# Optimization experiments

Measured on AMD Instinct MI355X. Metric: run time of the kernel, lower is better.

Reference implementation:

```python
import jax, jax.numpy as jnp
import numpy as np


def setup_inputs() -> dict:
    key = jax.random.key(0)
    k1, k2 = jax.random.split(key)
    s = jax.random.normal(k1, (8192, 512), dtype=jnp.float32)
    t = jax.random.normal(k2, (8192, 512), dtype=jnp.float32)
    return {"s": s, "t": t}


def reference(s, t):
    # Pairwise squared Euclidean distance: dist[i, j] = ||t[j] - s[i]||^2
    # Expressed via the identity ||s||^2 + ||t||^2 - 2 s @ t^T to avoid
    # materializing the [n, q, d] broadcast intermediate of the original.
    s_sq = jnp.sum(s * s, axis=1)  # [n]
    t_sq = jnp.sum(t * t, axis=1)  # [q]
    cross = jnp.einsum('nd,qd->nq', s, t)  # [n, q]
    dist = s_sq[:, None] + t_sq[None, :] - 2.0 * cross
    return dist
```

## Files before the change

### kernel.cpp

```cpp
#include <hip/hip_runtime.h>
#include <hip/hip_bf16.h>
#include <stdint.h>


typedef __attribute__((ext_vector_type(8))) short short8v;
typedef __attribute__((ext_vector_type(4))) float f32x4;

static __device__ __forceinline__ unsigned short f32_to_bf16_rne(float f) {
    unsigned int u = __float_as_uint(f);
    unsigned int lsb = (u >> 16) & 1u;
    u += 0x7fffu + lsb;
    return (unsigned short)(u >> 16);
}

static __device__ __forceinline__ void async_load16(const void* g, void* l) {
    __builtin_amdgcn_global_load_lds(
        (const __attribute__((address_space(1))) void*)g,
        (__attribute__((address_space(3))) void*)l,
        16, 0, 0);
}

__global__ __launch_bounds__(256) void prep_kernel(const float* __restrict__ x,
                                                   unsigned short* __restrict__ xb,
                                                   float* __restrict__ nrm,
                                                   float scale) {
    const int tid  = threadIdx.x;
    const int wid  = tid >> 6;
    const int lane = tid & 63;
    const int row  = blockIdx.x * 4 + wid;
    const float* xr = x + (size_t)row * 512;

    float4 v0 = ((const float4*)xr)[lane * 2 + 0];
    float4 v1 = ((const float4*)xr)[lane * 2 + 1];

    float ss = v0.x * v0.x + v0.y * v0.y + v0.z * v0.z + v0.w * v0.w
             + v1.x * v1.x + v1.y * v1.y + v1.z * v1.z + v1.w * v1.w;
#pragma unroll
    for (int off = 32; off > 0; off >>= 1) ss += __shfl_down(ss, off, 64);
    if (lane == 0) nrm[row] = ss;

    unsigned short u[8];
    float vals[8] = {v0.x, v0.y, v0.z, v0.w, v1.x, v1.y, v1.z, v1.w};
#pragma unroll
    for (int e = 0; e < 8; ++e) u[e] = f32_to_bf16_rne(vals[e] * scale);
    unsigned int w0 = (unsigned)u[0] | ((unsigned)u[1] << 16);
    unsigned int w1 = (unsigned)u[2] | ((unsigned)u[3] << 16);
    unsigned int w2 = (unsigned)u[4] | ((unsigned)u[5] << 16);
    unsigned int w3 = (unsigned)u[6] | ((unsigned)u[7] << 16);
    uint4 pk = make_uint4(w0, w1, w2, w3);
    ((uint4*)(xb + (size_t)row * 512))[lane] = pk;
}

#define TILE 128
#define BK 64

__global__ __launch_bounds__(256) void dist_mfma(const unsigned short* __restrict__ sb,
                                                 const unsigned short* __restrict__ tb,
                                                 const float* __restrict__ ssq,
                                                 const float* __restrict__ tsq,
                                                 float* __restrict__ out,
                                                 int N, int Q, int D) {
    __shared__ unsigned short lds_a[TILE * BK];
    __shared__ unsigned short lds_b[TILE * BK];

    const int tid  = threadIdx.x;
    const int wid  = tid >> 6;
    const int lane = tid & 63;
    const int quad = lane >> 4;
    const int r    = lane & 15;

    const int bid = blockIdx.x;
    const int nBm = N / TILE, nBn = Q / TILE;
    int bm, bn;
    if ((nBm & 7) == 0 && (nBn & 7) == 0) {
        const int super = bid >> 6, within = bid & 63;
        const int spr = nBn >> 3;
        const int sm = super / spr, sn = super % spr;
        bm = (sm << 3) + (within >> 3);
        bn = (sn << 3) + (within & 7);
    } else {
        bm = bid / nBn;
        bn = bid - bm * nBn;
    }

    const int m_w = (wid & 1) * 64;
    const int n_w = (wid >> 1) * 64;

    f32x4 acc[4][4];
#pragma unroll
    for (int a = 0; a < 4; ++a)
#pragma unroll
        for (int b = 0; b < 4; ++b) acc[a][b] = (f32x4){0.f, 0.f, 0.f, 0.f};

    const unsigned short* gA[4];
    const unsigned short* gB[4];
    unsigned short* lA[4];
    unsigned short* lB[4];
#pragma unroll
    for (int i = 0; i < 4; ++i) {
        const int p    = i * 256 + tid;
        const int row  = p >> 3;
        const int gch  = (tid & 7) ^ (row & 7);
        gA[i] = sb + (size_t)(bm * TILE + row) * D + gch * 8;
        gB[i] = tb + (size_t)(bn * TILE + row) * D + gch * 8;
        lA[i] = lds_a + (i * 256 + wid * 64) * 8;
        lB[i] = lds_b + (i * 256 + wid * 64) * 8;
    }

    for (int k0 = 0; k0 < D; k0 += BK) {
        __syncthreads();
#pragma unroll
        for (int i = 0; i < 4; ++i) {
            async_load16(gA[i] + k0, lA[i]);
            async_load16(gB[i] + k0, lB[i]);
        }
        __syncthreads();

#pragma unroll
        for (int ks = 0; ks < 2; ++ks) {
            short8v aF[4], bF[4];
#pragma unroll
            for (int im = 0; im < 4; ++im) {
                const int row = m_w + im * 16 + r;
                const int cp  = (ks * 4 + quad) ^ (row & 7);
                aF[im] = *(const short8v*)(lds_a + row * BK + cp * 8);
            }
#pragma unroll
            for (int in = 0; in < 4; ++in) {
                const int row = n_w + in * 16 + r;
                const int cp  = (ks * 4 + quad) ^ (row & 7);
                bF[in] = *(const short8v*)(lds_b + row * BK + cp * 8);
            }
#pragma unroll
            for (int im = 0; im < 4; ++im)
#pragma unroll
                for (int in = 0; in < 4; ++in)
                    acc[im][in] = __builtin_amdgcn_mfma_f32_16x16x32_bf16(
                        aF[im], bF[in], acc[im][in], 0, 0, 0);
        }
    }

    const int gm = bm * TILE + m_w;
    const int gn = bn * TILE + n_w;
    float tq[4];
#pragma unroll
    for (int in = 0; in < 4; ++in) tq[in] = tsq[gn + in * 16 + r];
#pragma unroll
    for (int im = 0; im < 4; ++im) {
#pragma unroll
        for (int j = 0; j < 4; ++j) {
            const int i = gm + im * 16 + quad * 4 + j;
            const float sv = ssq[i];
            float* orow = out + (size_t)i * (size_t)Q + gn;
#pragma unroll
            for (int in = 0; in < 4; ++in)
                __builtin_nontemporal_store(sv + tq[in] + acc[im][in][j],
                                            &orow[in * 16 + r]);
        }
    }
}

__global__ void dist_fallback(const float* __restrict__ s, const float* __restrict__ t,
                              float* __restrict__ out, int N, int Q, int D) {
    __shared__ float ls[16][17], lt[16][17];
    const int tj = threadIdx.x, ti = threadIdx.y;
    const int i = blockIdx.y * 16 + ti, j = blockIdx.x * 16 + tj;
    float cross = 0.f, ssq = 0.f, tsq = 0.f;
    for (int k0 = 0; k0 < D; k0 += 16) {
        __syncthreads();
        ls[ti][tj] = s[(size_t)(blockIdx.y * 16 + ti) * D + k0 + tj];
        lt[ti][tj] = t[(size_t)(blockIdx.x * 16 + ti) * D + k0 + tj];
        __syncthreads();
#pragma unroll
        for (int kk = 0; kk < 16; ++kk) {
            float a = ls[ti][kk], b = lt[tj][kk];
            cross += a * b; ssq += a * a; tsq += b * b;
        }
    }
    out[(size_t)i * Q + j] = ssq + tsq - 2.f * cross;
}

extern "C" void kernel_launch(void* const* d_in, const int* in_sizes, int n_in,
                              void* d_out, int out_size, void* d_ws, size_t ws_size,
                              hipStream_t stream) {
    const float* s = (const float*)d_in[0];
    const float* t = (const float*)d_in[1];
    float* out = (float*)d_out;
    const int D = 512;
    const int N = in_sizes[0] / D;
    const int Q = in_sizes[1] / D;

    const size_t need = ((size_t)N + (size_t)Q) * D * sizeof(unsigned short)
                      + ((size_t)N + (size_t)Q) * sizeof(float);

    if (ws_size >= need && D == 512 && (N % TILE) == 0 && (Q % TILE) == 0) {
        unsigned short* sb = (unsigned short*)d_ws;
        unsigned short* tb = sb + (size_t)N * D;
        float* ssq = (float*)(tb + (size_t)Q * D);
        float* tsq = ssq + N;
        prep_kernel<<<N / 4, 256, 0, stream>>>(s, sb, ssq, -2.0f);
        prep_kernel<<<Q / 4, 256, 0, stream>>>(t, tb, tsq, 1.0f);
        const int blocks = (N / TILE) * (Q / TILE);
        dist_mfma<<<blocks, 256, 0, stream>>>(sb, tb, ssq, tsq, out, N, Q, D);
    } else {
        dim3 g(Q / 16, N / 16), b(16, 16);
        dist_fallback<<<g, b, 0, stream>>>(s, t, out, N, Q, D);
    }
}
```

Baseline: 349.8 us.

## Double-buffer LDS k-tiles with async prefetch and merge prep launches

Result: slower. 366.1 us (+4.7%).

```diff
diff --git a/kernel.cpp b/kernel.cpp
--- a/kernel.cpp
+++ b/kernel.cpp
@@ -20,15 +20,23 @@
         16, 0, 0);
 }
 
-__global__ __launch_bounds__(256) void prep_kernel(const float* __restrict__ x,
-                                                   unsigned short* __restrict__ xb,
-                                                   float* __restrict__ nrm,
-                                                   float scale) {
+__global__ __launch_bounds__(256) void prep_kernel(const float* __restrict__ s,
+                                                   const float* __restrict__ t,
+                                                   unsigned short* __restrict__ sb,
+                                                   unsigned short* __restrict__ tb,
+                                                   float* __restrict__ snrm,
+                                                   float* __restrict__ tnrm,
+                                                   int N) {
     const int tid  = threadIdx.x;
     const int wid  = tid >> 6;
     const int lane = tid & 63;
-    const int row  = blockIdx.x * 4 + wid;
-    const float* xr = x + (size_t)row * 512;
+    const int g    = blockIdx.x * 4 + wid;
+    const bool is_s = (g < N);
+    const int row  = is_s ? g : g - N;
+    const float* xr = (is_s ? s : t) + (size_t)row * 512;
+    unsigned short* xb = (is_s ? sb : tb) + (size_t)row * 512;
+    float* nrm = is_s ? snrm : tnrm;
+    const float scale = is_s ? -2.0f : 1.0f;
 
     float4 v0 = ((const float4*)xr)[lane * 2 + 0];
     float4 v1 = ((const float4*)xr)[lane * 2 + 1];
@@ -47,12 +55,11 @@
     unsigned int w1 = (unsigned)u[2] | ((unsigned)u[3] << 16);
     unsigned int w2 = (unsigned)u[4] | ((unsigned)u[5] << 16);
     unsigned int w3 = (unsigned)u[6] | ((unsigned)u[7] << 16);
-    uint4 pk = make_uint4(w0, w1, w2, w3);
-    ((uint4*)(xb + (size_t)row * 512))[lane] = pk;
+    ((uint4*)xb)[lane] = make_uint4(w0, w1, w2, w3);
 }
 
 #define TILE 128
-#define BK 64
+#define BK 32
 
 __global__ __launch_bounds__(256) void dist_mfma(const unsigned short* __restrict__ sb,
                                                  const unsigned short* __restrict__ tb,
@@ -60,8 +67,8 @@
                                                  const float* __restrict__ tsq,
                                                  float* __restrict__ out,
                                                  int N, int Q, int D) {
-    __shared__ unsigned short lds_a[TILE * BK];
-    __shared__ unsigned short lds_b[TILE * BK];
+    __shared__ unsigned short lds_a[2][TILE * BK];
+    __shared__ unsigned short lds_b[2][TILE * BK];
 
     const int tid  = threadIdx.x;
     const int wid  = tid >> 6;
@@ -92,52 +99,64 @@
 #pragma unroll
         for (int b = 0; b < 4; ++b) acc[a][b] = (f32x4){0.f, 0.f, 0.f, 0.f};
 
-    const unsigned short* gA[4];
-    const unsigned short* gB[4];
-    unsigned short* lA[4];
-    unsigned short* lB[4];
-#pragma unroll
-    for (int i = 0; i < 4; ++i) {
-        const int p    = i * 256 + tid;
-        const int row  = p >> 3;
-        const int gch  = (tid & 7) ^ (row & 7);
-        gA[i] = sb + (size_t)(bm * TILE + row) * D + gch * 8;
-        gB[i] = tb + (size_t)(bn * TILE + row) * D + gch * 8;
-        lA[i] = lds_a + (i * 256 + wid * 64) * 8;
-        lB[i] = lds_b + (i * 256 + wid * 64) * 8;
-    }
-
-    for (int k0 = 0; k0 < D; k0 += BK) {
+    const unsigned short* gA[2];
+    const unsigned short* gB[2];
+    int lofs[2];
+#pragma unroll
+    for (int j = 0; j < 2; ++j) {
+        const int p   = j * 256 + tid;
+        const int row = p >> 2;
+        const int gch = (p & 3) ^ (row & 3);
+        gA[j] = sb + (size_t)(bm * TILE + row) * D + gch * 8;
+        gB[j] = tb + (size_t)(bn * TILE + row) * D + gch * 8;
+        lofs[j] = (j * 256 + wid * 64) * 8;
+    }
+
+    const int nIter = D / BK;
+
+#pragma unroll
+    for (int j = 0; j < 2; ++j) {
+        async_load16(gA[j], lds_a[0] + lofs[j]);
+        async_load16(gB[j], lds_b[0] + lofs[j]);
+    }
+    __syncthreads();
+
+    int aofs[4], bofs[4];
+#pragma unroll
+    for (int im = 0; im < 4; ++im) {
+        const int row = m_w + im * 16 + r;
+        aofs[im] = row * BK + ((quad ^ (row & 3)) * 8);
+    }
+#pragma unroll
+    for (int in = 0; in < 4; ++in) {
+        const int row = n_w + in * 16 + r;
+        bofs[in] = row * BK + ((quad ^ (row & 3)) * 8);
+    }
+
+    for (int k = 0; k < nIter; ++k) {
+        const int cur = k & 1, nxt = cur ^ 1;
+        if (k + 1 < nIter) {
+            const int k1 = (k + 1) * BK;
+#pragma unroll
+            for (int j = 0; j < 2; ++j) {
+                async_load16(gA[j] + k1, lds_a[nxt] + lofs[j]);
+                async_load16(gB[j] + k1, lds_b[nxt] + lofs[j]);
+            }
+        }
+        short8v aF[4], bF[4];
+#pragma unroll
+        for (int im = 0; im < 4; ++im)
+            aF[im] = *(const short8v*)(lds_a[cur] + aofs[im]);
+#pragma unroll
+        for (int in = 0; in < 4; ++in)
+            bF[in] = *(const short8v*)(lds_b[cur] + bofs[in]);
+#pragma unroll
+        for (int im = 0; im < 4; ++im)
+#pragma unroll
+            for (int in = 0; in < 4; ++in)
+                acc[im][in] = __builtin_amdgcn_mfma_f32_16x16x32_bf16(
+                    aF[im], bF[in], acc[im][in], 0, 0, 0);
         __syncthreads();
-#pragma unroll
-        for (int i = 0; i < 4; ++i) {
-            async_load16(gA[i] + k0, lA[i]);
-            async_load16(gB[i] + k0, lB[i]);
-        }
-        __syncthreads();
-
-#pragma unroll
-        for (int ks = 0; ks < 2; ++ks) {
-            short8v aF[4], bF[4];
-#pragma unroll
-            for (int im = 0; im < 4; ++im) {
-                const int row = m_w + im * 16 + r;
-                const int cp  = (ks * 4 + quad) ^ (row & 7);
-                aF[im] = *(const short8v*)(lds_a + row * BK + cp * 8);
-            }
-#pragma unroll
-            for (int in = 0; in < 4; ++in) {
-                const int row = n_w + in * 16 + r;
-                const int cp  = (ks * 4 + quad) ^ (row & 7);
-                bF[in] = *(const short8v*)(lds_b + row * BK + cp * 8);
-            }
-#pragma unroll
-            for (int im = 0; im < 4; ++im)
-#pragma unroll
-                for (int in = 0; in < 4; ++in)
-                    acc[im][in] = __builtin_amdgcn_mfma_f32_16x16x32_bf16(
-                        aF[im], bF[in], acc[im][in], 0, 0, 0);
-        }
     }
 
     const int gm = bm * TILE + m_w;
@@ -198,8 +217,7 @@
         unsigned short* tb = sb + (size_t)N * D;
         float* ssq = (float*)(tb + (size_t)Q * D);
         float* tsq = ssq + N;
-        prep_kernel<<<N / 4, 256, 0, stream>>>(s, sb, ssq, -2.0f);
-        prep_kernel<<<Q / 4, 256, 0, stream>>>(t, tb, tsq, 1.0f);
+        prep_kernel<<<(N + Q) / 4, 256, 0, stream>>>(s, t, sb, tb, ssq, tsq, N);
         const int blocks = (N / TILE) * (Q / TILE);
         dist_mfma<<<blocks, 256, 0, stream>>>(sb, tb, ssq, tsq, out, N, Q, D);
     } else {
```
